# Kernel optimization log

Hardware: AMD Instinct MI355X
Metric: run time of the kernel (lower is better)

The kernel has to match this reference:

```python
import jax, jax.numpy as jnp
import numpy as np

B, S, D = 64, 8192, 128  # batch, source length, hidden (enc == dec)


def setup_inputs() -> dict:
    key = jax.random.key(0)
    ks = jax.random.split(key, 7)
    s = 1.0 / np.sqrt(D)
    return {
        "input": jax.random.normal(ks[0], (B, D), jnp.float32),
        "context": jax.random.normal(ks[1], (B, S, D), jnp.float32),
        "W_enc": jax.random.uniform(ks[2], (D, D), jnp.float32, -s, s),
        "b_enc": jax.random.uniform(ks[3], (D,), jnp.float32, -s, s),
        "W_dec": jax.random.uniform(ks[4], (D, D), jnp.float32, -s, s),
        "b_dec": jax.random.uniform(ks[5], (D,), jnp.float32, -s, s),
        "W_out": jax.random.uniform(ks[6], (D, 2 * D), jnp.float32, -s, s),  # no bias
    }


def reference(input, context, W_enc, b_enc, W_dec, b_dec, W_out):
    # projected_context = tanh(lin_encoder(context))  [B, S, D]
    pc = jnp.tanh(jnp.einsum("bse,de->bsd", context, W_enc) + b_enc)
    # q = tanh(lin_decoder(input))  [B, D]
    q = jnp.tanh(input @ W_dec.T + b_dec)
    # attention scores via bmm(projected_context, q): [B, S]
    scores = jnp.einsum("bsd,bd->bs", pc, q)
    attn = jax.nn.softmax(scores, axis=1)  # softmax over source positions
    # weighted sum of (raw) context: [B, D]
    weighted_context = jnp.einsum("bs,bsd->bd", attn, context)
    # h_tilde = tanh(linear_out(concat(weighted_context, q)))  [B, D]
    h_tilde = jnp.tanh(jnp.concatenate([weighted_context, q], axis=-1) @ W_out.T)
    return h_tilde, attn
```

## Files before the change

kernel.cpp:

```cpp
#include <hip/hip_runtime.h>
#include <hip/hip_bf16.h>

#define BB 64
#define SS 8192
#define DD 128
#define NCHUNK 8
#define CHROWS 1024
#define NTILE 16

typedef __attribute__((ext_vector_type(8))) short bf16x8;
typedef __attribute__((ext_vector_type(4))) float f32x4;

#define SWZ(c, qd) ((qd) * 16 + ((c) ^ (2 * (qd))))

__device__ __forceinline__ unsigned pk2(float x, float y) {
    __hip_bfloat162 h = __float22bfloat162_rn(make_float2(x, y));
    union { __hip_bfloat162 h2; unsigned u; } cv;
    cv.h2 = h;
    return cv.u;
}

__device__ __forceinline__ float bflo(unsigned p) { return __uint_as_float(p << 16); }
__device__ __forceinline__ float bfhi(unsigned p) { return __uint_as_float(p & 0xffff0000u); }

__device__ __forceinline__ float tanh_fast(float x) {
    float e = __expf(2.f * x);
    return 1.f - 2.f / (e + 1.f);
}

__device__ __forceinline__ void lds_barrier() {
    asm volatile("s_waitcnt lgkmcnt(0)" ::: "memory");
    __builtin_amdgcn_s_barrier();
    asm volatile("" ::: "memory");
}

__global__ void qproj_kernel(const float* __restrict__ input,
                             const float* __restrict__ W_dec,
                             const float* __restrict__ b_dec,
                             float* __restrict__ q) {
    __shared__ float xin[DD];
    const int b = blockIdx.x, d = threadIdx.x;
    xin[d] = input[b * DD + d];
    __syncthreads();
    const float4* wrow = (const float4*)(W_dec + (size_t)d * DD);
    float acc = 0.f;
#pragma unroll
    for (int k4 = 0; k4 < DD / 4; k4++) {
        float4 w = wrow[k4];
        float4 x = ((const float4*)xin)[k4];
        acc += w.x * x.x + w.y * x.y + w.z * x.z + w.w * x.w;
    }
    q[b * DD + d] = tanh_fast(acc + b_dec[d]);
}

__global__ __launch_bounds__(256, 2) void score_fused_kernel(
    const float* __restrict__ ctx,
    const float* __restrict__ W_enc,
    const float* __restrict__ b_enc,
    const float* __restrict__ q,
    float* __restrict__ scores,
    float* __restrict__ wcp,
    float* __restrict__ Mp,
    float* __restrict__ Tp) {
    __shared__ __align__(16) short Wl[16384];
    __shared__ __align__(16) short Cl[2][8192];
    __shared__ float sw[64];
    __shared__ float4 red[256];

    const int t = threadIdx.x;

    const float4* W4 = (const float4*)W_enc;
    for (int c2 = t; c2 < 2048; c2 += 256) {
        int row = c2 >> 4, kc = c2 & 15;
        float4 f0 = W4[row * 32 + kc * 2];
        float4 f1 = W4[row * 32 + kc * 2 + 1];
        int nt = row >> 4, colw = row & 15, kk = kc >> 2, qd = kc & 3;
        int a8 = (nt * 4 + kk) * 128 + SWZ(colw, qd) * 2;
        uint4 u;
        u.x = pk2(f0.x, f0.y); u.y = pk2(f0.z, f0.w);
        u.z = pk2(f1.x, f1.y); u.w = pk2(f1.z, f1.w);
        *(uint4*)&Wl[a8 * 4] = u;
    }

    const int wv = t >> 6, lane = t & 63;
    const int col = lane & 15, quad = lane >> 4;
    const int b = blockIdx.x >> 3;
    const int chunk = blockIdx.x & 7;

    const int u = t & 31, rg = t >> 5;
    const int ukk = u >> 3, uqd = (u >> 1) & 3, uh = u & 1;

    float qv[8], bv[8];
#pragma unroll
    for (int nt = 0; nt < 8; nt++) {
        qv[nt] = q[b * DD + nt * 16 + col];
        bv[nt] = b_enc[nt * 16 + col];
    }

    const float4* base = (const float4*)(ctx + ((size_t)b * SS + (size_t)chunk * CHROWS) * DD);

    float4 R[8];
    uint2 P[8];
    auto pack_tile = [&](int buf) {
#pragma unroll
        for (int i = 0; i < 8; i++) {
            int row = rg + 8 * i, w = row >> 4, c = row & 15;
            int a8 = (w * 4 + ukk) * 128 + SWZ(c, uqd) * 2 + uh;
            uint2 pk;
            pk.x = pk2(R[i].x, R[i].y);
            pk.y = pk2(R[i].z, R[i].w);
            P[i] = pk;
            *(uint2*)&Cl[buf][a8 * 4] = pk;
        }
    };

#pragma unroll
    for (int i = 0; i < 8; i++) R[i] = base[t + 256 * i];
    pack_tile(0);
    __syncthreads();

    float Mrun = -INFINITY, Trun = 0.f;
    float4 acc4 = {0.f, 0.f, 0.f, 0.f};

    for (int it = 0; it < NTILE; ++it) {
        const int cur = it & 1;
        if (it < NTILE - 1) {
            const float4* tb = base + (size_t)(it + 1) * 2048;
#pragma unroll
            for (int i = 0; i < 8; i++) R[i] = tb[t + 256 * i];
        }

        bf16x8 a[4];
#pragma unroll
        for (int kk = 0; kk < 4; kk++) {
            int a8 = (wv * 4 + kk) * 128 + SWZ(col, quad) * 2;
            a[kk] = *(const bf16x8*)&Cl[cur][a8 * 4];
        }
        f32x4 acc[8];
#pragma unroll
        for (int nt = 0; nt < 8; nt++) {
            f32x4 c = {0.f, 0.f, 0.f, 0.f};
#pragma unroll
            for (int kk = 0; kk < 4; kk++) {
                int a8 = (nt * 4 + kk) * 128 + SWZ(col, quad) * 2;
                bf16x8 bf = *(const bf16x8*)&Wl[a8 * 4];
                c = __builtin_amdgcn_mfma_f32_16x16x32_bf16(a[kk], bf, c, 0, 0, 0);
            }
            acc[nt] = c;
        }

#pragma unroll
        for (int r = 0; r < 4; r++) {
            float v = 0.f;
#pragma unroll
            for (int nt = 0; nt < 8; nt++)
                v += tanh_fast(acc[nt][r] + bv[nt]) * qv[nt];
            v += __shfl_xor(v, 1);
            v += __shfl_xor(v, 2);
            v += __shfl_xor(v, 4);
            v += __shfl_xor(v, 8);
            if (col == 0) {
                int lrow = wv * 16 + quad * 4 + r;
                sw[lrow] = v;
                scores[(size_t)b * SS + (size_t)chunk * CHROWS + it * 64 + lrow] = v;
            }
        }
        lds_barrier();

        float sv = sw[lane];
        float m = sv;
#pragma unroll
        for (int off = 1; off < 64; off <<= 1) m = fmaxf(m, __shfl_xor(m, off));
        float Mnew = fmaxf(Mrun, m);
        float alpha = __expf(Mrun - Mnew);
        float wlane = __expf(sv - Mnew);
        float ts = wlane;
#pragma unroll
        for (int off = 1; off < 64; off <<= 1) ts += __shfl_xor(ts, off);
        Trun = Trun * alpha + ts;
        Mrun = Mnew;

        acc4.x *= alpha; acc4.y *= alpha; acc4.z *= alpha; acc4.w *= alpha;
#pragma unroll
        for (int i = 0; i < 8; i++) {
            int row = rg + 8 * i;
            uint2 pk = P[i];
            float wi = __shfl(wlane, row);
            acc4.x += wi * bflo(pk.x);
            acc4.y += wi * bfhi(pk.x);
            acc4.z += wi * bflo(pk.y);
            acc4.w += wi * bfhi(pk.y);
        }

        if (it < NTILE - 1) pack_tile(cur ^ 1);

        lds_barrier();
    }

    red[t] = acc4;
    __syncthreads();
    if (t < 32) {
        float4 s = red[t];
#pragma unroll
        for (int k = 1; k < 8; k++) {
            float4 p = red[t + 32 * k];
            s.x += p.x; s.y += p.y; s.z += p.z; s.w += p.w;
        }
        *(float4*)&wcp[(size_t)blockIdx.x * DD + 4 * t] = s;
    }
    if (t == 0) {
        Mp[blockIdx.x] = Mrun;
        Tp[blockIdx.x] = Trun;
    }
}

__global__ void combine_out_kernel(const float* __restrict__ wcp,
                                   const float* __restrict__ Mp,
                                   const float* __restrict__ Tp,
                                   const float* __restrict__ q,
                                   const float* __restrict__ W_out,
                                   float* __restrict__ h,
                                   float* __restrict__ Ms,
                                   float* __restrict__ Tinv) {
    __shared__ float cat[2 * DD];
    const int b = blockIdx.x, d = threadIdx.x;
    float M = -INFINITY;
#pragma unroll
    for (int j = 0; j < NCHUNK; j++) M = fmaxf(M, Mp[b * NCHUNK + j]);
    float T = 0.f, acc = 0.f;
#pragma unroll
    for (int j = 0; j < NCHUNK; j++) {
        float e = __expf(Mp[b * NCHUNK + j] - M);
        T += Tp[b * NCHUNK + j] * e;
        acc += wcp[(size_t)(b * NCHUNK + j) * DD + d] * e;
    }
    float ti = 1.f / T;
    cat[d] = acc * ti;
    cat[DD + d] = q[b * DD + d];
    if (d == 0) { Ms[b] = M; Tinv[b] = ti; }
    __syncthreads();
    const float4* wrow = (const float4*)(W_out + (size_t)d * 2 * DD);
    float a2 = 0.f;
#pragma unroll
    for (int k4 = 0; k4 < 2 * DD / 4; k4++) {
        float4 w = wrow[k4];
        float4 x = ((const float4*)cat)[k4];
        a2 += w.x * x.x + w.y * x.y + w.z * x.z + w.w * x.w;
    }
    h[b * DD + d] = tanh_fast(a2);
}

__global__ __launch_bounds__(512) void attnfin_kernel(const float* __restrict__ scores,
                                                      const float* __restrict__ Ms,
                                                      const float* __restrict__ Tinv,
                                                      float* __restrict__ attn) {
    const int b = blockIdx.x >> 2, seg = blockIdx.x & 3;
    const float M = Ms[b], ti = Tinv[b];
    const float4* s4 = (const float4*)(scores + (size_t)b * SS) + seg * 512;
    float4* a4 = (float4*)(attn + (size_t)b * SS) + seg * 512;
    float4 v = s4[threadIdx.x];
    v.x = __expf(v.x - M) * ti;
    v.y = __expf(v.y - M) * ti;
    v.z = __expf(v.z - M) * ti;
    v.w = __expf(v.w - M) * ti;
    a4[threadIdx.x] = v;
}

extern "C" void kernel_launch(void* const* d_in, const int* in_sizes, int n_in,
                              void* d_out, int out_size, void* d_ws, size_t ws_size,
                              hipStream_t stream) {
    const float* input = (const float*)d_in[0];
    const float* ctx   = (const float*)d_in[1];
    const float* W_enc = (const float*)d_in[2];
    const float* b_enc = (const float*)d_in[3];
    const float* W_dec = (const float*)d_in[4];
    const float* b_dec = (const float*)d_in[5];
    const float* W_out = (const float*)d_in[6];

    float* h    = (float*)d_out;
    float* attn = (float*)d_out + BB * DD;

    float* ws     = (float*)d_ws;
    float* q      = ws;
    float* scores = ws + 8192;
    float* wcp    = scores + 524288;
    float* Mp     = wcp + 512 * DD;
    float* Tp     = Mp + 512;
    float* Ms     = Tp + 512;
    float* Tinv   = Ms + 64;

    qproj_kernel<<<BB, DD, 0, stream>>>(input, W_dec, b_dec, q);
    score_fused_kernel<<<BB * NCHUNK, 256, 0, stream>>>(ctx, W_enc, b_enc, q,
                                                        scores, wcp, Mp, Tp);
    combine_out_kernel<<<BB, DD, 0, stream>>>(wcp, Mp, Tp, q, W_out, h, Ms, Tinv);
    attnfin_kernel<<<BB * 4, 512, 0, stream>>>(scores, Ms, Tinv, attn);
}
```

Measured before the change: 400.7 us.

## Fuse decoder query projection into score kernel and decouple attn finalize

Removes the separate q-projection kernel: each score block now computes tanh(W_dec·input+b_dec) for its batch row into shared memory, with chunk 0 also writing q out for the combine kernel. attnfin now derives the softmax max and normalizer itself from the per-chunk partials, so it no longer depends on combine_out and Ms/Tinv are dropped. This cuts one launch and the serial dependency between kernels. The cost is redundant q computation across the 8 chunk blocks and 8x redundant W_dec reads, which adds some work to the prologue of the main kernel.

```diff
diff --git a/kernel.cpp b/kernel.cpp
--- a/kernel.cpp
+++ b/kernel.cpp
@@ -34,30 +34,14 @@
     asm volatile("" ::: "memory");
 }
 
-__global__ void qproj_kernel(const float* __restrict__ input,
-                             const float* __restrict__ W_dec,
-                             const float* __restrict__ b_dec,
-                             float* __restrict__ q) {
-    __shared__ float xin[DD];
-    const int b = blockIdx.x, d = threadIdx.x;
-    xin[d] = input[b * DD + d];
-    __syncthreads();
-    const float4* wrow = (const float4*)(W_dec + (size_t)d * DD);
-    float acc = 0.f;
-#pragma unroll
-    for (int k4 = 0; k4 < DD / 4; k4++) {
-        float4 w = wrow[k4];
-        float4 x = ((const float4*)xin)[k4];
-        acc += w.x * x.x + w.y * x.y + w.z * x.z + w.w * x.w;
-    }
-    q[b * DD + d] = tanh_fast(acc + b_dec[d]);
-}
-
 __global__ __launch_bounds__(256, 2) void score_fused_kernel(
     const float* __restrict__ ctx,
     const float* __restrict__ W_enc,
     const float* __restrict__ b_enc,
-    const float* __restrict__ q,
+    const float* __restrict__ input,
+    const float* __restrict__ W_dec,
+    const float* __restrict__ b_dec,
+    float* __restrict__ q,
     float* __restrict__ scores,
     float* __restrict__ wcp,
     float* __restrict__ Mp,
@@ -66,8 +50,14 @@
     __shared__ __align__(16) short Cl[2][8192];
     __shared__ float sw[64];
     __shared__ float4 red[256];
+    __shared__ float xin[DD];
+    __shared__ float qsh[DD];
 
     const int t = threadIdx.x;
+    const int b = blockIdx.x >> 3;
+    const int chunk = blockIdx.x & 7;
+
+    if (t < DD) xin[t] = input[b * DD + t];
 
     const float4* W4 = (const float4*)W_enc;
     for (int c2 = t; c2 < 2048; c2 += 256) {
@@ -84,18 +74,9 @@
 
     const int wv = t >> 6, lane = t & 63;
     const int col = lane & 15, quad = lane >> 4;
-    const int b = blockIdx.x >> 3;
-    const int chunk = blockIdx.x & 7;
 
     const int u = t & 31, rg = t >> 5;
     const int ukk = u >> 3, uqd = (u >> 1) & 3, uh = u & 1;
-
-    float qv[8], bv[8];
-#pragma unroll
-    for (int nt = 0; nt < 8; nt++) {
-        qv[nt] = q[b * DD + nt * 16 + col];
-        bv[nt] = b_enc[nt * 16 + col];
-    }
 
     const float4* base = (const float4*)(ctx + ((size_t)b * SS + (size_t)chunk * CHROWS) * DD);
 
@@ -116,8 +97,31 @@
 
 #pragma unroll
     for (int i = 0; i < 8; i++) R[i] = base[t + 256 * i];
+
+    __syncthreads();
+
+    if (t < DD) {
+        const float4* wrow = (const float4*)(W_dec + (size_t)t * DD);
+        float acc = 0.f;
+#pragma unroll
+        for (int k4 = 0; k4 < DD / 4; k4++) {
+            float4 w = wrow[k4];
+            float4 x = ((const float4*)xin)[k4];
+            acc += w.x * x.x + w.y * x.y + w.z * x.z + w.w * x.w;
+        }
+        float qs = tanh_fast(acc + b_dec[t]);
+        qsh[t] = qs;
+        if (chunk == 0) q[b * DD + t] = qs;
+    }
     pack_tile(0);
     __syncthreads();
+
+    float qv[8], bv[8];
+#pragma unroll
+    for (int nt = 0; nt < 8; nt++) {
+        qv[nt] = qsh[nt * 16 + col];
+        bv[nt] = b_enc[nt * 16 + col];
+    }
 
     float Mrun = -INFINITY, Trun = 0.f;
     float4 acc4 = {0.f, 0.f, 0.f, 0.f};
@@ -219,9 +223,7 @@
                                    const float* __restrict__ Tp,
                                    const float* __restrict__ q,
                                    const float* __restrict__ W_out,
-                                   float* __restrict__ h,
-                                   float* __restrict__ Ms,
-                                   float* __restrict__ Tinv) {
+                                   float* __restrict__ h) {
     __shared__ float cat[2 * DD];
     const int b = blockIdx.x, d = threadIdx.x;
     float M = -INFINITY;
@@ -237,7 +239,6 @@
     float ti = 1.f / T;
     cat[d] = acc * ti;
     cat[DD + d] = q[b * DD + d];
-    if (d == 0) { Ms[b] = M; Tinv[b] = ti; }
     __syncthreads();
     const float4* wrow = (const float4*)(W_out + (size_t)d * 2 * DD);
     float a2 = 0.f;
@@ -251,11 +252,17 @@
 }
 
 __global__ __launch_bounds__(512) void attnfin_kernel(const float* __restrict__ scores,
-                                                      const float* __restrict__ Ms,
-                                                      const float* __restrict__ Tinv,
+                                                      const float* __restrict__ Mp,
+                                                      const float* __restrict__ Tp,
                                                       float* __restrict__ attn) {
     const int b = blockIdx.x >> 2, seg = blockIdx.x & 3;
-    const float M = Ms[b], ti = Tinv[b];
+    float M = -INFINITY;
+#pragma unroll
+    for (int j = 0; j < NCHUNK; j++) M = fmaxf(M, Mp[b * NCHUNK + j]);
+    float T = 0.f;
+#pragma unroll
+    for (int j = 0; j < NCHUNK; j++) T += Tp[b * NCHUNK + j] * __expf(Mp[b * NCHUNK + j] - M);
+    const float ti = 1.f / T;
     const float4* s4 = (const float4*)(scores + (size_t)b * SS) + seg * 512;
     float4* a4 = (float4*)(attn + (size_t)b * SS) + seg * 512;
     float4 v = s4[threadIdx.x];
@@ -286,12 +293,10 @@
     float* wcp    = scores + 524288;
     float* Mp     = wcp + 512 * DD;
     float* Tp     = Mp + 512;
-    float* Ms     = Tp + 512;
-    float* Tinv   = Ms + 64;
-
-    qproj_kernel<<<BB, DD, 0, stream>>>(input, W_dec, b_dec, q);
-    score_fused_kernel<<<BB * NCHUNK, 256, 0, stream>>>(ctx, W_enc, b_enc, q,
-                                                        scores, wcp, Mp, Tp);
-    combine_out_kernel<<<BB, DD, 0, stream>>>(wcp, Mp, Tp, q, W_out, h, Ms, Tinv);
-    attnfin_kernel<<<BB * 4, 512, 0, stream>>>(scores, Ms, Tinv, attn);
-}
+
+    score_fused_kernel<<<BB * NCHUNK, 256, 0, stream>>>(ctx, W_enc, b_enc,
+                                                        input, W_dec, b_dec,
+                                                        q, scores, wcp, Mp, Tp);
+    attnfin_kernel<<<BB * 4, 512, 0, stream>>>(scores, Mp, Tp, attn);
+    combine_out_kernel<<<BB, DD, 0, stream>>>(wcp, Mp, Tp, q, W_out, h);
+}
```

Result: no change. 401.9 us (+0.3%).
